# Kernel optimization log

Hardware: AMD Instinct MI355X
Metric: run time of the kernel (lower is better)

## Reference

```python
import jax, jax.numpy as jnp
import numpy as np

NUM_HEADS = 16
BLOCK = 64  # block_size = min(64, N)

def setup_inputs() -> dict:
    key = jax.random.key(0)
    k0, k1, k2 = jax.random.split(key, 3)
    B, N, C = 2, 2048, 1024
    x = jax.random.normal(k0, (B, N, C), dtype=jnp.float32)
    w_qkv = jax.random.normal(k1, (3 * C, C), dtype=jnp.float32) * 0.02  # torch Linear weight [out,in]
    w_proj = jax.random.normal(k2, (C, C), dtype=jnp.float32) * 0.02
    b_proj = jnp.zeros((C,), dtype=jnp.float32)
    return {"x": x, "w_qkv": w_qkv, "w_proj": w_proj, "b_proj": b_proj}

def reference(x, w_qkv, w_proj, b_proj):
    B, N, C = x.shape
    H = NUM_HEADS
    hd = C // H
    bs = min(BLOCK, N)
    scale = hd ** -0.5
    # qkv projection: [B,N,3C] -> [3,B,H,N,hd]
    qkv = (x @ w_qkv.T).reshape(B, N, 3, H, hd).transpose(2, 0, 3, 1, 4)
    q, k, v = qkv[0], qkv[1], qkv[2]
    # block-causal mask: query block i attends to all key blocks <= i
    blk = jnp.arange(N) // bs
    mask = blk[:, None] >= blk[None, :]  # [N,N]
    scores = jnp.einsum('bhqd,bhkd->bhqk', q, k) * scale
    scores = jnp.where(mask, scores, -jnp.inf)
    weights = jax.nn.softmax(scores, axis=-1)
    out = jnp.einsum('bhqk,bhkd->bhqd', weights, v)
    out = out.transpose(0, 2, 1, 3).reshape(B, N, C)
    return out @ w_proj.T + b_proj
```

## Files before the change

kernel.cpp:

```cpp
#include <hip/hip_runtime.h>

typedef __attribute__((ext_vector_type(8))) short bf16x8;
typedef __attribute__((ext_vector_type(4))) float f32x4;

__device__ __forceinline__ unsigned short f2bf(float f) {
  unsigned int u = __float_as_uint(f);
  u += 0x7fffu + ((u >> 16) & 1u);
  return (unsigned short)(u >> 16);
}

__device__ __forceinline__ void gload_lds16(const unsigned short* g, unsigned short* l) {
  __builtin_amdgcn_global_load_lds(
      (const __attribute__((address_space(1))) unsigned int*)g,
      (__attribute__((address_space(3))) unsigned int*)l,
      16, 0, 0);
}

__global__ void cvt_bf16_kernel(const float* __restrict__ src,
                                unsigned short* __restrict__ dst, int n) {
  int stride = gridDim.x * blockDim.x;
  for (int i = blockIdx.x * blockDim.x + threadIdx.x; i * 4 < n; i += stride) {
    float4 v = *(const float4*)(src + (size_t)i * 4);
    ushort4 o;
    o.x = f2bf(v.x); o.y = f2bf(v.y); o.z = f2bf(v.z); o.w = f2bf(v.w);
    *(ushort4*)(dst + (size_t)i * 4) = o;
  }
}

__device__ __forceinline__ void gemm128_bt(const unsigned short* __restrict__ A,
                                           const unsigned short* __restrict__ Bt,
                                           unsigned short* As, unsigned short* Bs,
                                           int tm, int tn, f32x4 acc[4][4]) {
  const int K = 1024;
  int tid = threadIdx.x;
  int w = tid >> 6, l = tid & 63;
  int wr = w >> 1, wc = w & 1;
  int g = l >> 4, c = l & 15;

  int srow = w * 32 + (l >> 2);
  int skoff = (l & 3) * 8;
  const unsigned short* gA = A + (size_t)(tm * 128 + srow) * K + skoff;
  const unsigned short* gB = Bt + (size_t)(tn * 128 + srow) * K + skoff;
  unsigned short* lA = As + (w * 32) * 32;
  unsigned short* lB = Bs + (w * 32) * 32;

  for (int k0 = 0; k0 < K; k0 += 32) {
    gload_lds16(gA, lA);
    gload_lds16(gA + 16 * K, lA + 16 * 32);
    gload_lds16(gB, lB);
    gload_lds16(gB + 16 * K, lB + 16 * 32);
    gA += 32; gB += 32;
    __syncthreads();
    bf16x8 af[4], bfr[4];
#pragma unroll
    for (int mi = 0; mi < 4; ++mi)
      af[mi] = *(const bf16x8*)(As + (wr * 64 + mi * 16 + c) * 32 + 8 * g);
#pragma unroll
    for (int ni = 0; ni < 4; ++ni)
      bfr[ni] = *(const bf16x8*)(Bs + (wc * 64 + ni * 16 + c) * 32 + 8 * g);
#pragma unroll
    for (int mi = 0; mi < 4; ++mi)
#pragma unroll
      for (int ni = 0; ni < 4; ++ni)
        acc[mi][ni] = __builtin_amdgcn_mfma_f32_16x16x32_bf16(af[mi], bfr[ni], acc[mi][ni], 0, 0, 0);
    __syncthreads();
  }
}

__global__ __launch_bounds__(256) void qkv_gemm(const unsigned short* __restrict__ xb,
                                                const unsigned short* __restrict__ wb,
                                                unsigned short* __restrict__ Qp,
                                                unsigned short* __restrict__ Kp,
                                                unsigned short* __restrict__ Vt) {
  __shared__ unsigned short As[128 * 32];
  __shared__ unsigned short Bs[128 * 32];
  f32x4 acc[4][4];
#pragma unroll
  for (int i = 0; i < 4; ++i)
#pragma unroll
    for (int j = 0; j < 4; ++j) acc[i][j] = f32x4{0.f, 0.f, 0.f, 0.f};
  int tm = blockIdx.y, tn = blockIdx.x;
  gemm128_bt(xb, wb, As, Bs, tm, tn, acc);

  int tid = threadIdx.x;
  int w = tid >> 6, l = tid & 63;
  int wr = w >> 1, wc = w & 1;
  int g = l >> 4, c = l & 15;
  const float QSCALE = 0.125f * 1.44269504088896f;
#pragma unroll
  for (int mi = 0; mi < 4; ++mi)
#pragma unroll
    for (int ni = 0; ni < 4; ++ni)
#pragma unroll
      for (int r = 0; r < 4; ++r) {
        int row = tm * 128 + wr * 64 + mi * 16 + g * 4 + r;
        int col = tn * 128 + wc * 64 + ni * 16 + c;
        int b = row >> 11, seq = row & 2047;
        int t = col >> 10;
        int h = (col >> 6) & 15, d = col & 63;
        size_t bh = (size_t)b * 16 + h;
        float v = acc[mi][ni][r];
        if (t == 0)      Qp[(bh * 2048 + seq) * 64 + d] = f2bf(v * QSCALE);
        else if (t == 1) Kp[(bh * 2048 + seq) * 64 + d] = f2bf(v);
        else             Vt[(bh * 64 + d) * 2048 + seq] = f2bf(v);
      }
}

__global__ __launch_bounds__(256, 3) void attn_fa(const unsigned short* __restrict__ Qp,
                                                  const unsigned short* __restrict__ Kp,
                                                  const unsigned short* __restrict__ Vt,
                                                  unsigned short* __restrict__ attn) {
  __shared__ unsigned short Ks[2][4096];
  __shared__ unsigned short Vs[2][4096];
  __shared__ unsigned short Plds[4][16][72];
  int tid = threadIdx.x;
  int w = tid >> 6, l = tid & 63;
  int g = l >> 4, c = l & 15;

  int idx = blockIdx.x;
  int pos = idx >> 3;
  int qb = 31 - (pos >> 2);
  int bh = (idx & 7) + 8 * (pos & 3);

  const unsigned short* Qbh = Qp + (size_t)bh * 2048 * 64;
  const unsigned short* Kbh = Kp + (size_t)bh * 2048 * 64;
  const unsigned short* Vbh = Vt + (size_t)bh * 64 * 2048;

  int rowA, colA, rowB, colB;
  { int L = tid * 16;         int P = L ^ (((L >> 7) & 7) << 4); rowA = P >> 7; colA = (P & 127) >> 1; }
  { int L = (tid + 256) * 16; int P = L ^ (((L >> 7) & 7) << 4); rowB = P >> 7; colB = (P & 127) >> 1; }
  const unsigned short* gKA = Kbh + rowA * 64 + colA;
  const unsigned short* gKB = Kbh + rowB * 64 + colB;
  const unsigned short* gVA = Vbh + (size_t)rowA * 2048 + colA;
  const unsigned short* gVB = Vbh + (size_t)rowB * 2048 + colB;

#define STAGE(buf, kb)                                              \
  do {                                                              \
    gload_lds16(gKA + (kb) * 4096, &Ks[(buf)][w * 512]);            \
    gload_lds16(gKB + (kb) * 4096, &Ks[(buf)][w * 512 + 2048]);     \
    gload_lds16(gVA + (kb) * 64,  &Vs[(buf)][w * 512]);             \
    gload_lds16(gVB + (kb) * 64,  &Vs[(buf)][w * 512 + 2048]);      \
  } while (0)

  bf16x8 qf[2];
  {
    size_t qrow = (size_t)qb * 64 + w * 16 + c;
    qf[0] = *(const bf16x8*)(Qbh + qrow * 64 + 8 * g);
    qf[1] = *(const bf16x8*)(Qbh + qrow * 64 + 32 + 8 * g);
  }

  float lp[4] = {0.f, 0.f, 0.f, 0.f};
  f32x4 o[4];
#pragma unroll
  for (int df = 0; df < 4; ++df) o[df] = f32x4{0.f, 0.f, 0.f, 0.f};

  int xorv = c & 7;

  int cur = 0;
  STAGE(0, 0);
  __syncthreads();
  for (int kb = 0; kb <= qb; ++kb) {
    if (kb < qb) STAGE(1 - cur, kb + 1);

    const char* Kb = (const char*)&Ks[cur][0];
    const char* Vb = (const char*)&Vs[cur][0];
    bf16x8 kf[8];
#pragma unroll
    for (int nf = 0; nf < 4; ++nf) {
      int r = nf * 16 + c;
#pragma unroll
      for (int ks = 0; ks < 2; ++ks)
        kf[nf * 2 + ks] = *(const bf16x8*)(Kb + r * 128 + (((ks * 4 + g) ^ xorv) * 16));
    }
    f32x4 s4[4];
#pragma unroll
    for (int nf = 0; nf < 4; ++nf) {
      s4[nf] = f32x4{0.f, 0.f, 0.f, 0.f};
      s4[nf] = __builtin_amdgcn_mfma_f32_16x16x32_bf16(qf[0], kf[nf * 2 + 0], s4[nf], 0, 0, 0);
      s4[nf] = __builtin_amdgcn_mfma_f32_16x16x32_bf16(qf[1], kf[nf * 2 + 1], s4[nf], 0, 0, 0);
    }
    bf16x8 vf[8];
#pragma unroll
    for (int df = 0; df < 4; ++df) {
      int r = df * 16 + c;
#pragma unroll
      for (int ks = 0; ks < 2; ++ks)
        vf[df * 2 + ks] = *(const bf16x8*)(Vb + r * 128 + (((ks * 4 + g) ^ xorv) * 16));
    }
#pragma unroll
    for (int nf = 0; nf < 4; ++nf)
#pragma unroll
      for (int r = 0; r < 4; ++r) {
        float p = __builtin_amdgcn_exp2f(s4[nf][r]);
        lp[r] += p;
        Plds[w][g * 4 + r][nf * 16 + c] = f2bf(p);
      }
#pragma unroll
    for (int ks = 0; ks < 2; ++ks) {
      bf16x8 pf = *(const bf16x8*)(&Plds[w][c][ks * 32 + 8 * g]);
#pragma unroll
      for (int df = 0; df < 4; ++df)
        o[df] = __builtin_amdgcn_mfma_f32_16x16x32_bf16(pf, vf[df * 2 + ks], o[df], 0, 0, 0);
    }
    __syncthreads();
    cur ^= 1;
  }
#undef STAGE

#pragma unroll
  for (int mask = 1; mask < 16; mask <<= 1)
#pragma unroll
    for (int r = 0; r < 4; ++r) lp[r] += __shfl_xor(lp[r], mask);

  int b = bh >> 4, h = bh & 15;
#pragma unroll
  for (int df = 0; df < 4; ++df)
#pragma unroll
    for (int r = 0; r < 4; ++r) {
      int row = qb * 64 + w * 16 + g * 4 + r;
      int colc = h * 64 + df * 16 + c;
      attn[((size_t)b * 2048 + row) * 1024 + colc] = f2bf(o[df][r] / lp[r]);
    }
}

__global__ __launch_bounds__(256) void proj_gemm(const unsigned short* __restrict__ attn,
                                                 const unsigned short* __restrict__ wpb,
                                                 const float* __restrict__ bias,
                                                 float* __restrict__ out) {
  __shared__ unsigned short As[128 * 32];
  __shared__ unsigned short Bs[128 * 32];
  f32x4 acc[4][4];
#pragma unroll
  for (int i = 0; i < 4; ++i)
#pragma unroll
    for (int j = 0; j < 4; ++j) acc[i][j] = f32x4{0.f, 0.f, 0.f, 0.f};
  int tm = blockIdx.y, tn = blockIdx.x;
  gemm128_bt(attn, wpb, As, Bs, tm, tn, acc);

  int tid = threadIdx.x;
  int w = tid >> 6, l = tid & 63;
  int wr = w >> 1, wc = w & 1;
  int g = l >> 4, c = l & 15;
#pragma unroll
  for (int mi = 0; mi < 4; ++mi)
#pragma unroll
    for (int ni = 0; ni < 4; ++ni)
#pragma unroll
      for (int r = 0; r < 4; ++r) {
        int row = tm * 128 + wr * 64 + mi * 16 + g * 4 + r;
        int col = tn * 128 + wc * 64 + ni * 16 + c;
        out[(size_t)row * 1024 + col] = acc[mi][ni][r] + bias[col];
      }
}

extern "C" void kernel_launch(void* const* d_in, const int* in_sizes, int n_in,
                              void* d_out, int out_size, void* d_ws, size_t ws_size,
                              hipStream_t stream) {
  (void)in_sizes; (void)n_in; (void)out_size; (void)ws_size;
  const float* x      = (const float*)d_in[0];
  const float* w_qkv  = (const float*)d_in[1];
  const float* w_proj = (const float*)d_in[2];
  const float* b_proj = (const float*)d_in[3];
  float* out = (float*)d_out;

  unsigned short* xb    = (unsigned short*)d_ws;
  unsigned short* wqkvb = xb + 4096 * 1024;
  unsigned short* wpb   = wqkvb + 3072 * 1024;
  unsigned short* Qp    = wpb + 1024 * 1024;
  unsigned short* Kp    = Qp + 32 * 2048 * 64;
  unsigned short* Vt    = Kp + 32 * 2048 * 64;
  unsigned short* attn  = Vt + 32 * 64 * 2048;

  cvt_bf16_kernel<<<1024, 256, 0, stream>>>(x, xb, 4096 * 1024);
  cvt_bf16_kernel<<<1024, 256, 0, stream>>>(w_qkv, wqkvb, 3072 * 1024);
  cvt_bf16_kernel<<<512, 256, 0, stream>>>(w_proj, wpb, 1024 * 1024);
  qkv_gemm<<<dim3(24, 32), 256, 0, stream>>>(xb, wqkvb, Qp, Kp, Vt);
  attn_fa<<<1024, 256, 0, stream>>>(Qp, Kp, Vt, attn);
  proj_gemm<<<dim3(8, 32), 256, 0, stream>>>(attn, wpb, b_proj, out);
}
```

Before: 119.8 us.

## Swizzle GEMM LDS tiles, remap blocks across XCDs, fuse conversions, use rcp

The change XOR-swizzles the 16-byte k-chunks of the GEMM LDS tiles so that the MFMA fragment reads avoid bank conflicts. It remaps the 1D grid of block IDs so that consecutive tiles land on the same XCD, which should improve L2 reuse. It merges the three fp32-to-bf16 conversion launches into one kernel, removing two launches. The attention epilogue now multiplies by a hardware reciprocal instead of dividing, at a slight cost in precision.

```diff
diff --git a/kernel.cpp b/kernel.cpp
--- a/kernel.cpp
+++ b/kernel.cpp
@@ -16,14 +16,19 @@
       16, 0, 0);
 }
 
-__global__ void cvt_bf16_kernel(const float* __restrict__ src,
-                                unsigned short* __restrict__ dst, int n) {
+__global__ void cvt_all(const float* __restrict__ x, const float* __restrict__ wq,
+                        const float* __restrict__ wp, unsigned short* __restrict__ dst) {
+  const int n1 = 4096 * 1024 / 4, n2 = 3072 * 1024 / 4, n3 = 1024 * 1024 / 4;
   int stride = gridDim.x * blockDim.x;
-  for (int i = blockIdx.x * blockDim.x + threadIdx.x; i * 4 < n; i += stride) {
-    float4 v = *(const float4*)(src + (size_t)i * 4);
+  for (int i = blockIdx.x * blockDim.x + threadIdx.x; i < n1 + n2 + n3; i += stride) {
+    const float* s; int j;
+    if (i < n1)           { s = x;  j = i; }
+    else if (i < n1 + n2) { s = wq; j = i - n1; }
+    else                  { s = wp; j = i - n1 - n2; }
+    float4 v = ((const float4*)s)[j];
     ushort4 o;
     o.x = f2bf(v.x); o.y = f2bf(v.y); o.z = f2bf(v.z); o.w = f2bf(v.w);
-    *(ushort4*)(dst + (size_t)i * 4) = o;
+    ((ushort4*)dst)[i] = o;
   }
 }
 
@@ -38,11 +43,15 @@
   int g = l >> 4, c = l & 15;
 
   int srow = w * 32 + (l >> 2);
-  int skoff = (l & 3) * 8;
+  int skoff = (((l & 3) ^ ((srow >> 1) & 3)) * 8);
   const unsigned short* gA = A + (size_t)(tm * 128 + srow) * K + skoff;
   const unsigned short* gB = Bt + (size_t)(tn * 128 + srow) * K + skoff;
   unsigned short* lA = As + (w * 32) * 32;
   unsigned short* lB = Bs + (w * 32) * 32;
+
+  int rx = (c >> 1) & 3;
+  int arow = wr * 64 + c;
+  int brow = wc * 64 + c;
 
   for (int k0 = 0; k0 < K; k0 += 32) {
     gload_lds16(gA, lA);
@@ -54,10 +63,10 @@
     bf16x8 af[4], bfr[4];
 #pragma unroll
     for (int mi = 0; mi < 4; ++mi)
-      af[mi] = *(const bf16x8*)(As + (wr * 64 + mi * 16 + c) * 32 + 8 * g);
+      af[mi] = *(const bf16x8*)((const char*)As + (arow + mi * 16) * 64 + ((g ^ rx) << 4));
 #pragma unroll
     for (int ni = 0; ni < 4; ++ni)
-      bfr[ni] = *(const bf16x8*)(Bs + (wc * 64 + ni * 16 + c) * 32 + 8 * g);
+      bfr[ni] = *(const bf16x8*)((const char*)Bs + (brow + ni * 16) * 64 + ((g ^ rx) << 4));
 #pragma unroll
     for (int mi = 0; mi < 4; ++mi)
 #pragma unroll
@@ -79,7 +88,8 @@
   for (int i = 0; i < 4; ++i)
 #pragma unroll
     for (int j = 0; j < 4; ++j) acc[i][j] = f32x4{0.f, 0.f, 0.f, 0.f};
-  int tm = blockIdx.y, tn = blockIdx.x;
+  int id = (blockIdx.x & 7) * 96 + (blockIdx.x >> 3);
+  int tm = id / 24, tn = id % 24;
   gemm128_bt(xb, wb, As, Bs, tm, tn, acc);
 
   int tid = threadIdx.x;
@@ -211,6 +221,9 @@
   for (int mask = 1; mask < 16; mask <<= 1)
 #pragma unroll
     for (int r = 0; r < 4; ++r) lp[r] += __shfl_xor(lp[r], mask);
+  float inv[4];
+#pragma unroll
+  for (int r = 0; r < 4; ++r) inv[r] = __builtin_amdgcn_rcpf(lp[r]);
 
   int b = bh >> 4, h = bh & 15;
 #pragma unroll
@@ -219,7 +232,7 @@
     for (int r = 0; r < 4; ++r) {
       int row = qb * 64 + w * 16 + g * 4 + r;
       int colc = h * 64 + df * 16 + c;
-      attn[((size_t)b * 2048 + row) * 1024 + colc] = f2bf(o[df][r] / lp[r]);
+      attn[((size_t)b * 2048 + row) * 1024 + colc] = f2bf(o[df][r] * inv[r]);
     }
 }
 
@@ -234,7 +247,8 @@
   for (int i = 0; i < 4; ++i)
 #pragma unroll
     for (int j = 0; j < 4; ++j) acc[i][j] = f32x4{0.f, 0.f, 0.f, 0.f};
-  int tm = blockIdx.y, tn = blockIdx.x;
+  int id = (blockIdx.x & 7) * 32 + (blockIdx.x >> 3);
+  int tm = id / 8, tn = id % 8;
   gemm128_bt(attn, wpb, As, Bs, tm, tn, acc);
 
   int tid = threadIdx.x;
@@ -271,10 +285,8 @@
   unsigned short* Vt    = Kp + 32 * 2048 * 64;
   unsigned short* attn  = Vt + 32 * 64 * 2048;
 
-  cvt_bf16_kernel<<<1024, 256, 0, stream>>>(x, xb, 4096 * 1024);
-  cvt_bf16_kernel<<<1024, 256, 0, stream>>>(w_qkv, wqkvb, 3072 * 1024);
-  cvt_bf16_kernel<<<512, 256, 0, stream>>>(w_proj, wpb, 1024 * 1024);
-  qkv_gemm<<<dim3(24, 32), 256, 0, stream>>>(xb, wqkvb, Qp, Kp, Vt);
+  cvt_all<<<2048, 256, 0, stream>>>(x, w_qkv, w_proj, xb);
+  qkv_gemm<<<768, 256, 0, stream>>>(xb, wqkvb, Qp, Kp, Vt);
   attn_fa<<<1024, 256, 0, stream>>>(Qp, Kp, Vt, attn);
-  proj_gemm<<<dim3(8, 32), 256, 0, stream>>>(attn, wpb, b_proj, out);
-}
+  proj_gemm<<<256, 256, 0, stream>>>(attn, wpb, b_proj, out);
+}
```

Result: faster. 112.3 us (-6.2%).
